# Kernel optimization log

Hardware: AMD Instinct MI355X
Metric: run time of the kernel (lower is better)

The kernel has to match this reference:

```python
import jax, jax.numpy as jnp
import numpy as np
import math

B, S, E, H = 4, 4096, 2048, 16
Dh = E // H  # 128


def setup_inputs() -> dict:
    key = jax.random.key(0)
    ks = jax.random.split(key, 8)
    s = 1.0 / math.sqrt(E)
    return {
        "x": jax.random.normal(ks[0], (B, S, E), dtype=jnp.float32),
        "Wz": jax.random.uniform(ks[1], (E, E), jnp.float32, -s, s),
        "bz": jax.random.uniform(ks[2], (E,), jnp.float32, -s, s),
        "Wx": jax.random.uniform(ks[3], (E, E), jnp.float32, -s, s),
        "bx": jax.random.uniform(ks[4], (E,), jnp.float32, -s, s),
        "phase": jax.random.normal(ks[5], (H, Dh), dtype=jnp.float32),
        "Wo": jax.random.uniform(ks[6], (E, E), jnp.float32, -s, s),
        "bo": jax.random.uniform(ks[7], (E,), jnp.float32, -s, s),
    }


def reference(x, Wz, bz, Wx, bx, phase, Wo, bo):
    # torch nn.Linear: y = x @ W.T + b  (W stored [out, in])
    z = x @ Wz.T + bz                     # [B,S,E]
    xs = x @ Wx.T + bx                    # [B,S,E]
    z_h = z.reshape(B, S, H, Dh)
    x_h = xs.reshape(B, S, H, Dh)
    # elementwise phase modulation of query heads
    mod = z_h * jnp.sin(phase)            # [B,S,H,Dh] * [H,Dh]
    # NOTE: heads are on axis -2 (no transpose to [B,H,S,Dh]),
    # so scores contract over Dh giving per-token HEAD-mixing: [B,S,H,H]
    scores = jnp.einsum('bshd,bsgd->bshg', mod, x_h) / math.sqrt(Dh)
    w = jax.nn.softmax(scores, axis=-1)   # softmax over head axis g
    att = jnp.einsum('bshg,bsgd->bshd', w, x_h)  # [B,S,H,Dh]
    att = att.reshape(B, S, E)
    return att @ Wo.T + bo
```

## Files before the change

kernel.cpp:

```cpp
#include <hip/hip_runtime.h>
#include <hip/hip_bf16.h>

#define TOK 16384
#define E 2048
#define DH 128

using bf16x8 = __attribute__((ext_vector_type(8))) __bf16;
using f32x4  = __attribute__((ext_vector_type(4))) float;
using u16x8  = __attribute__((ext_vector_type(8))) unsigned short;

static __device__ __forceinline__ unsigned short f2bf(float f) {
  union { float f; unsigned u; } x; x.f = f;
  unsigned r = x.u + 0x7fffu + ((x.u >> 16) & 1u);
  return (unsigned short)(r >> 16);
}

static __device__ __forceinline__ void gload_lds16(const unsigned short* g, unsigned short* l) {
  __builtin_amdgcn_global_load_lds(
      (const __attribute__((address_space(1))) void*)g,
      (__attribute__((address_space(3))) void*)l, 16, 0, 0);
}

__global__ __launch_bounds__(256) void cvt_plain(const float* __restrict__ in,
                                                 unsigned short* __restrict__ out, int n8) {
  int stride = gridDim.x * blockDim.x;
  for (int i = blockIdx.x * blockDim.x + threadIdx.x; i < n8; i += stride) {
    const float4* p = reinterpret_cast<const float4*>(in) + (size_t)i * 2;
    float4 v0 = p[0], v1 = p[1];
    u16x8 o;
    o[0] = f2bf(v0.x); o[1] = f2bf(v0.y); o[2] = f2bf(v0.z); o[3] = f2bf(v0.w);
    o[4] = f2bf(v1.x); o[5] = f2bf(v1.y); o[6] = f2bf(v1.z); o[7] = f2bf(v1.w);
    *(reinterpret_cast<u16x8*>(out) + i) = o;
  }
}

__global__ __launch_bounds__(256) void cvt_scaled(const float* __restrict__ in,
                                                  const float* __restrict__ phase,
                                                  unsigned short* __restrict__ out, int n8) {
  const float rs = 0.08838834764831845f;
  int stride = gridDim.x * blockDim.x;
  for (int i = blockIdx.x * blockDim.x + threadIdx.x; i < n8; i += stride) {
    int row = i >> 8;
    float sc = sinf(phase[row]) * rs;
    const float4* p = reinterpret_cast<const float4*>(in) + (size_t)i * 2;
    float4 v0 = p[0], v1 = p[1];
    u16x8 o;
    o[0] = f2bf(v0.x * sc); o[1] = f2bf(v0.y * sc); o[2] = f2bf(v0.z * sc); o[3] = f2bf(v0.w * sc);
    o[4] = f2bf(v1.x * sc); o[5] = f2bf(v1.y * sc); o[6] = f2bf(v1.z * sc); o[7] = f2bf(v1.w * sc);
    *(reinterpret_cast<u16x8*>(out) + i) = o;
  }
}

__global__ __launch_bounds__(256) void scale_bias2(const float* __restrict__ bz,
                                                   const float* __restrict__ bx,
                                                   const float* __restrict__ phase,
                                                   float* __restrict__ out) {
  const float rs = 0.08838834764831845f;
  int i = blockIdx.x * blockDim.x + threadIdx.x;
  if (i < E) out[i] = bz[i] * sinf(phase[i]) * rs;
  else if (i < 2 * E) out[i] = bx[i - E];
}

#define MFMA16 __builtin_amdgcn_mfma_f32_16x16x32_bf16

static __device__ __forceinline__ bf16x8 ldf(const unsigned short* buf, int row, int slot) {
  return *reinterpret_cast<const bf16x8*>(buf + row * 64 + ((slot ^ (row & 7)) << 3));
}

static __device__ __forceinline__ void stage_half(const unsigned short* gbase, int ld,
                                                  unsigned short* dsthalf,
                                                  int r, int slot, int wave) {
#pragma unroll
  for (int c = 0; c < 2; ++c)
    gload_lds16(gbase + (size_t)(c * 64 + r) * ld + slot * 8,
                dsthalf + c * 4096 + wave * 512);
}

static __device__ __forceinline__ void quad(f32x4 (&acc)[8][4], const bf16x8 (&a)[4][2],
                                            const bf16x8 (&b)[2][2], int mh, int nh) {
#pragma unroll
  for (int mi = 0; mi < 4; ++mi)
#pragma unroll
    for (int ni = 0; ni < 2; ++ni)
#pragma unroll
      for (int kk = 0; kk < 2; ++kk)
        acc[mh * 4 + mi][nh * 2 + ni] =
            MFMA16(a[mi][kk], b[ni][kk], acc[mh * 4 + mi][nh * 2 + ni], 0, 0, 0);
}

#define PH_BAR()  __builtin_amdgcn_s_barrier()
#define VMCNT(n)  asm volatile("s_waitcnt vmcnt(" #n ")" ::: "memory")
#define PRIO1()   __builtin_amdgcn_s_setprio(1)
#define PRIO0()   __builtin_amdgcn_s_setprio(0)

#define LD_A(dst, buf, base)                                             \
  _Pragma("unroll")                                                      \
  for (int mi = 0; mi < 4; ++mi)                                         \
    _Pragma("unroll")                                                    \
    for (int kk = 0; kk < 2; ++kk)                                       \
      dst[mi][kk] = ldf(buf, (base) + mi * 16, kk * 4 + grp);

#define LD_B(dst, buf, base)                                             \
  _Pragma("unroll")                                                      \
  for (int ni = 0; ni < 2; ++ni)                                         \
    _Pragma("unroll")                                                    \
    for (int kk = 0; kk < 2; ++kk)                                       \
      dst[ni][kk] = ldf(buf, (base) + ni * 16, kk * 4 + grp);

template <bool LAST>
static __device__ __forceinline__ void k_iter(
    const unsigned short* __restrict__ Ag, const unsigned short* __restrict__ Bg,
    int K_, int lda, int t,
    unsigned short* sA0, unsigned short* sA1, unsigned short* sB0, unsigned short* sB1,
    int r, int slot, int wave, int grp, int rA, int rB,
    bf16x8 (&bP)[2][2], bf16x8 (&bQ)[2][2], f32x4 (&acc)[8][4]) {
  const size_t k1 = (size_t)(t + 1) * 64, k2 = (size_t)(t + 2) * 64, k3 = (size_t)(t + 3) * 64;
  const size_t hA = (size_t)128 * lda, hB = (size_t)128 * K_;
  bf16x8 aF[4][2], b1F[2][2];

  LD_A(aF, sA0, rA);
  stage_half(Ag + k1, lda, sA1, r, slot, wave);
  PRIO1(); quad(acc, aF, bP, 0, 0); PRIO0();
  LD_B(b1F, sB0, rB + 32);
  stage_half(Ag + hA + k1, lda, sA1 + 8192, r, slot, wave);
  PRIO1(); quad(acc, aF, b1F, 0, 1); PRIO0();
  VMCNT(4);
  PH_BAR();

  LD_A(aF, sA0, rA + 64);
  if (!LAST) stage_half(Bg + k2, K_, sB0, r, slot, wave);
  PRIO1(); quad(acc, aF, b1F, 1, 1); PRIO0();
  LD_B(bQ, sB1, rB);
  if (!LAST) stage_half(Bg + hB + k2, K_, sB0 + 8192, r, slot, wave);
  PRIO1(); quad(acc, aF, bP, 1, 0); PRIO0();
  if (!LAST) { VMCNT(4); } else { VMCNT(0); }
  PH_BAR();

  LD_A(aF, sA1, rA);
  if (!LAST) stage_half(Ag + k2, lda, sA0, r, slot, wave);
  PRIO1(); quad(acc, aF, bQ, 0, 0); PRIO0();
  LD_B(b1F, sB1, rB + 32);
  if (!LAST) stage_half(Ag + hA + k2, lda, sA0 + 8192, r, slot, wave);
  PRIO1(); quad(acc, aF, b1F, 0, 1); PRIO0();
  if (!LAST) { VMCNT(4); }
  PH_BAR();

  LD_A(aF, sA1, rA + 64);
  if (!LAST) stage_half(Bg + k3, K_, sB1, r, slot, wave);
  PRIO1(); quad(acc, aF, b1F, 1, 1); PRIO0();
  if (!LAST) {
    LD_B(bP, sB0, rB);
    stage_half(Bg + hB + k3, K_, sB1 + 8192, r, slot, wave);
  }
  PRIO1(); quad(acc, aF, bQ, 1, 0); PRIO0();
  if (!LAST) { VMCNT(4); }
  PH_BAR();
}

template <bool OUT_BF16>
__global__ __launch_bounds__(512, 2) void gemm256(const unsigned short* __restrict__ A,
                                                  const unsigned short* __restrict__ Bm,
                                                  const float* __restrict__ bias,
                                                  void* __restrict__ C,
                                                  int M, int N, int K_, int lda) {
  extern __shared__ unsigned short lds[];
  unsigned short* sA0 = lds;
  unsigned short* sA1 = lds + 16384;
  unsigned short* sB0 = lds + 32768;
  unsigned short* sB1 = lds + 49152;

  const int nbn = N >> 8;
  const int bid = blockIdx.x;
  const int swz = (bid & 7) * ((int)gridDim.x >> 3) + (bid >> 3);
  const int by = swz / nbn, bx = swz % nbn;
  const int tm = by << 8, tn = bx << 8;

  const int tid = threadIdx.x;
  const int wave = tid >> 6, lane = tid & 63;
  const int g16 = lane & 15, grp = lane >> 4;
  const int wm = wave >> 2, wn = wave & 3;
  const int rA = wm * 128 + g16;
  const int rB = wn * 64 + g16;
  const int r = tid >> 3;
  const int slot = (tid & 7) ^ ((tid >> 3) & 7);

  const unsigned short* Ag = A + (size_t)tm * lda;
  const unsigned short* Bg = Bm + (size_t)tn * K_;
  const size_t hA = (size_t)128 * lda, hB = (size_t)128 * K_;

  f32x4 acc[8][4];
#pragma unroll
  for (int i = 0; i < 8; ++i)
#pragma unroll
    for (int j = 0; j < 4; ++j) acc[i][j] = (f32x4){0.f, 0.f, 0.f, 0.f};

  bf16x8 bP[2][2], bQ[2][2];

  stage_half(Ag, lda, sA0, r, slot, wave);
  stage_half(Ag + hA, lda, sA0 + 8192, r, slot, wave);
  stage_half(Bg, K_, sB0, r, slot, wave);
  stage_half(Bg + hB, K_, sB0 + 8192, r, slot, wave);
  stage_half(Bg + 64, K_, sB1, r, slot, wave);
  stage_half(Bg + hB + 64, K_, sB1 + 8192, r, slot, wave);
  VMCNT(4);
  __builtin_amdgcn_s_barrier();
  LD_B(bP, sB0, rB);

  const int NI = K_ >> 7;
#pragma unroll 1
  for (int i = 0; i < NI - 1; ++i)
    k_iter<false>(Ag, Bg, K_, lda, 2 * i, sA0, sA1, sB0, sB1, r, slot, wave, grp, rA, rB,
                  bP, bQ, acc);
  k_iter<true>(Ag, Bg, K_, lda, 2 * (NI - 1), sA0, sA1, sB0, sB1, r, slot, wave, grp, rA, rB,
               bP, bQ, acc);

#pragma unroll
  for (int mi = 0; mi < 8; ++mi) {
#pragma unroll
    for (int ni = 0; ni < 4; ++ni) {
      const int row = tm + wm * 128 + mi * 16 + grp * 4;
      const int col = tn + wn * 64 + ni * 16 + g16;
      const float bv = bias[col];
#pragma unroll
      for (int j = 0; j < 4; ++j) {
        const float v = acc[mi][ni][j] + bv;
        if (OUT_BF16)
          ((unsigned short*)C)[(size_t)(row + j) * N + col] = f2bf(v);
        else
          ((float*)C)[(size_t)(row + j) * N + col] = v;
      }
    }
  }
}

__global__ __launch_bounds__(256) void attn_kernel(unsigned short* zc) {
  __shared__ __align__(16) unsigned short xs_lds[4][16][136];
  __shared__ float w_lds[4][16][17];

  const int wave = threadIdx.x >> 6, lane = threadIdx.x & 63;
  const int token = (blockIdx.x << 2) | wave;
  unsigned short* modp = zc + (size_t)token * (2 * E);
  const unsigned short* xsp = modp + E;
  const int g16 = lane & 15, grp = lane >> 4;

  bf16x8 a[4], b[4];
#pragma unroll
  for (int kk = 0; kk < 4; ++kk) {
    a[kk] = *reinterpret_cast<const bf16x8*>(modp + g16 * DH + kk * 32 + grp * 8);
    b[kk] = *reinterpret_cast<const bf16x8*>(xsp  + g16 * DH + kk * 32 + grp * 8);
  }
#pragma unroll
  for (int kk = 0; kk < 4; ++kk)
    *reinterpret_cast<bf16x8*>(&xs_lds[wave][g16][kk * 32 + grp * 8]) = b[kk];

  f32x4 sc = (f32x4){0.f, 0.f, 0.f, 0.f};
#pragma unroll
  for (int kk = 0; kk < 4; ++kk)
    sc = MFMA16(a[kk], b[kk], sc, 0, 0, 0);

  float w4[4];
#pragma unroll
  for (int j = 0; j < 4; ++j) {
    float s = sc[j];
    float m = s;
#pragma unroll
    for (int off = 1; off < 16; off <<= 1) m = fmaxf(m, __shfl_xor(m, off));
    float e = __expf(s - m);
    float t = e;
#pragma unroll
    for (int off = 1; off < 16; off <<= 1) t += __shfl_xor(t, off);
    w4[j] = e / t;
  }
#pragma unroll
  for (int j = 0; j < 4; ++j) w_lds[wave][grp * 4 + j][g16] = w4[j];

  __syncthreads();

  float acc[32];
#pragma unroll
  for (int i = 0; i < 32; ++i) acc[i] = 0.f;
#pragma unroll
  for (int g = 0; g < 16; ++g) {
    const float wg = w_lds[wave][g16][g];
#pragma unroll
    for (int c = 0; c < 4; ++c) {
      bf16x8 xv = *reinterpret_cast<const bf16x8*>(&xs_lds[wave][g][grp * 32 + c * 8]);
#pragma unroll
      for (int j = 0; j < 8; ++j) acc[c * 8 + j] += wg * (float)xv[j];
    }
  }

  unsigned short* op = modp + g16 * DH + grp * 32;
#pragma unroll
  for (int c = 0; c < 4; ++c) {
    u16x8 o;
#pragma unroll
    for (int j = 0; j < 8; ++j) o[j] = f2bf(acc[c * 8 + j]);
    *reinterpret_cast<u16x8*>(op + c * 8) = o;
  }
}

extern "C" void kernel_launch(void* const* d_in, const int* in_sizes, int n_in,
                              void* d_out, int out_size, void* d_ws, size_t ws_size,
                              hipStream_t stream) {
  const float* x     = (const float*)d_in[0];
  const float* Wz    = (const float*)d_in[1];
  const float* bz    = (const float*)d_in[2];
  const float* Wx    = (const float*)d_in[3];
  const float* bx    = (const float*)d_in[4];
  const float* phase = (const float*)d_in[5];
  const float* Wo    = (const float*)d_in[6];
  const float* bo    = (const float*)d_in[7];

  char* p = (char*)d_ws;
  unsigned short* x_bf  = (unsigned short*)p; p += (size_t)TOK * E * 2;
  unsigned short* C12   = (unsigned short*)p; p += (size_t)TOK * 2 * E * 2;
  unsigned short* wzx   = (unsigned short*)p; p += (size_t)2 * E * E * 2;
  unsigned short* wo_bf = (unsigned short*)p; p += (size_t)E * E * 2;
  float* bzx            = (float*)p;          p += (size_t)2 * E * 4;

  hipFuncSetAttribute((const void*)gemm256<true>,
                      hipFuncAttributeMaxDynamicSharedMemorySize, 131072);
  hipFuncSetAttribute((const void*)gemm256<false>,
                      hipFuncAttributeMaxDynamicSharedMemorySize, 131072);

  cvt_plain<<<2048, 256, 0, stream>>>(x, x_bf, TOK * E / 8);
  cvt_scaled<<<1024, 256, 0, stream>>>(Wz, phase, wzx, E * E / 8);
  cvt_plain<<<1024, 256, 0, stream>>>(Wx, wzx + (size_t)E * E, E * E / 8);
  cvt_plain<<<1024, 256, 0, stream>>>(Wo, wo_bf, E * E / 8);
  scale_bias2<<<2 * E / 256, 256, 0, stream>>>(bz, bx, phase, bzx);

  gemm256<true><<<dim3((TOK / 256) * (2 * E / 256)), 512, 131072, stream>>>(
      x_bf, wzx, bzx, C12, TOK, 2 * E, E, E);
  attn_kernel<<<TOK / 4, 256, 0, stream>>>(C12);
  gemm256<false><<<dim3((TOK / 256) * (E / 256)), 512, 131072, stream>>>(
      C12, wo_bf, bo, (float*)d_out, TOK, E, E, 2 * E);
}
```

Measured before the change: 454.5 us.

## Shrink GEMM tiles to 256x128 with K=32 stages and 4 waves

```diff
diff --git a/kernel.cpp b/kernel.cpp
--- a/kernel.cpp
+++ b/kernel.cpp
@@ -63,29 +63,28 @@
 
 #define MFMA16 __builtin_amdgcn_mfma_f32_16x16x32_bf16
 
-static __device__ __forceinline__ bf16x8 ldf(const unsigned short* buf, int row, int slot) {
-  return *reinterpret_cast<const bf16x8*>(buf + row * 64 + ((slot ^ (row & 7)) << 3));
-}
-
-static __device__ __forceinline__ void stage_half(const unsigned short* gbase, int ld,
-                                                  unsigned short* dsthalf,
-                                                  int r, int slot, int wave) {
-#pragma unroll
-  for (int c = 0; c < 2; ++c)
-    gload_lds16(gbase + (size_t)(c * 64 + r) * ld + slot * 8,
-                dsthalf + c * 4096 + wave * 512);
-}
-
-static __device__ __forceinline__ void quad(f32x4 (&acc)[8][4], const bf16x8 (&a)[4][2],
-                                            const bf16x8 (&b)[2][2], int mh, int nh) {
+static __device__ __forceinline__ bf16x8 ldf32(const unsigned short* buf, int row, int slot) {
+  return *reinterpret_cast<const bf16x8*>(buf + row * 32 + ((slot ^ (row & 3)) << 3));
+}
+
+template <int NCH>
+static __device__ __forceinline__ void stage_tile(const unsigned short* gbase, int ld,
+                                                  unsigned short* dst,
+                                                  int srow, int s0, int wave) {
+#pragma unroll
+  for (int c = 0; c < NCH; ++c)
+    gload_lds16(gbase + (size_t)(c * 64 + srow) * ld + s0 * 8,
+                dst + c * 2048 + wave * 512);
+}
+
+static __device__ __forceinline__ void q8(f32x4 (&acc)[8][4], const bf16x8 (&a)[4],
+                                          const bf16x8 (&b)[2], int mh, int nh) {
 #pragma unroll
   for (int mi = 0; mi < 4; ++mi)
 #pragma unroll
     for (int ni = 0; ni < 2; ++ni)
-#pragma unroll
-      for (int kk = 0; kk < 2; ++kk)
-        acc[mh * 4 + mi][nh * 2 + ni] =
-            MFMA16(a[mi][kk], b[ni][kk], acc[mh * 4 + mi][nh * 2 + ni], 0, 0, 0);
+      acc[mh * 4 + mi][nh * 2 + ni] =
+          MFMA16(a[mi], b[ni], acc[mh * 4 + mi][nh * 2 + ni], 0, 0, 0);
 }
 
 #define PH_BAR()  __builtin_amdgcn_s_barrier()
@@ -93,100 +92,82 @@
 #define PRIO1()   __builtin_amdgcn_s_setprio(1)
 #define PRIO0()   __builtin_amdgcn_s_setprio(0)
 
-#define LD_A(dst, buf, base)                                             \
+#define LDA32(dst, buf, base)                                            \
   _Pragma("unroll")                                                      \
   for (int mi = 0; mi < 4; ++mi)                                         \
-    _Pragma("unroll")                                                    \
-    for (int kk = 0; kk < 2; ++kk)                                       \
-      dst[mi][kk] = ldf(buf, (base) + mi * 16, kk * 4 + grp);
-
-#define LD_B(dst, buf, base)                                             \
+    dst[mi] = ldf32(buf, (base) + mi * 16, grp);
+
+#define LDB32(dst, buf, base)                                            \
   _Pragma("unroll")                                                      \
   for (int ni = 0; ni < 2; ++ni)                                         \
-    _Pragma("unroll")                                                    \
-    for (int kk = 0; kk < 2; ++kk)                                       \
-      dst[ni][kk] = ldf(buf, (base) + ni * 16, kk * 4 + grp);
+    dst[ni] = ldf32(buf, (base) + ni * 16, grp);
 
 template <bool LAST>
 static __device__ __forceinline__ void k_iter(
     const unsigned short* __restrict__ Ag, const unsigned short* __restrict__ Bg,
     int K_, int lda, int t,
     unsigned short* sA0, unsigned short* sA1, unsigned short* sB0, unsigned short* sB1,
-    int r, int slot, int wave, int grp, int rA, int rB,
-    bf16x8 (&bP)[2][2], bf16x8 (&bQ)[2][2], f32x4 (&acc)[8][4]) {
-  const size_t k1 = (size_t)(t + 1) * 64, k2 = (size_t)(t + 2) * 64, k3 = (size_t)(t + 3) * 64;
-  const size_t hA = (size_t)128 * lda, hB = (size_t)128 * K_;
-  bf16x8 aF[4][2], b1F[2][2];
-
-  LD_A(aF, sA0, rA);
-  stage_half(Ag + k1, lda, sA1, r, slot, wave);
-  PRIO1(); quad(acc, aF, bP, 0, 0); PRIO0();
-  LD_B(b1F, sB0, rB + 32);
-  stage_half(Ag + hA + k1, lda, sA1 + 8192, r, slot, wave);
-  PRIO1(); quad(acc, aF, b1F, 0, 1); PRIO0();
-  VMCNT(4);
+    int srow, int s0, int wave, int grp, int rA, int rB, f32x4 (&acc)[8][4]) {
+  const size_t k1 = (size_t)(t + 1) * 32, k2 = (size_t)(t + 2) * 32, k3 = (size_t)(t + 3) * 32;
+  bf16x8 aF[4], b0[2], b1[2];
+
+  LDA32(aF, sA0, rA);
+  LDB32(b0, sB0, rB);
+  LDB32(b1, sB0, rB + 32);
+  stage_tile<4>(Ag + k1, lda, sA1, srow, s0, wave);
+  PRIO1(); q8(acc, aF, b0, 0, 0); q8(acc, aF, b1, 0, 1); PRIO0();
   PH_BAR();
 
-  LD_A(aF, sA0, rA + 64);
-  if (!LAST) stage_half(Bg + k2, K_, sB0, r, slot, wave);
-  PRIO1(); quad(acc, aF, b1F, 1, 1); PRIO0();
-  LD_B(bQ, sB1, rB);
-  if (!LAST) stage_half(Bg + hB + k2, K_, sB0 + 8192, r, slot, wave);
-  PRIO1(); quad(acc, aF, bP, 1, 0); PRIO0();
-  if (!LAST) { VMCNT(4); } else { VMCNT(0); }
+  LDA32(aF, sA0, rA + 64);
+  if (!LAST) stage_tile<2>(Bg + k2, K_, sB0, srow, s0, wave);
+  PRIO1(); q8(acc, aF, b1, 1, 1); q8(acc, aF, b0, 1, 0); PRIO0();
+  if (!LAST) { VMCNT(2); } else { VMCNT(0); }
   PH_BAR();
 
-  LD_A(aF, sA1, rA);
-  if (!LAST) stage_half(Ag + k2, lda, sA0, r, slot, wave);
-  PRIO1(); quad(acc, aF, bQ, 0, 0); PRIO0();
-  LD_B(b1F, sB1, rB + 32);
-  if (!LAST) stage_half(Ag + hA + k2, lda, sA0 + 8192, r, slot, wave);
-  PRIO1(); quad(acc, aF, b1F, 0, 1); PRIO0();
-  if (!LAST) { VMCNT(4); }
+  LDA32(aF, sA1, rA);
+  LDB32(b0, sB1, rB);
+  LDB32(b1, sB1, rB + 32);
+  if (!LAST) stage_tile<4>(Ag + k2, lda, sA0, srow, s0, wave);
+  PRIO1(); q8(acc, aF, b0, 0, 0); q8(acc, aF, b1, 0, 1); PRIO0();
   PH_BAR();
 
-  LD_A(aF, sA1, rA + 64);
-  if (!LAST) stage_half(Bg + k3, K_, sB1, r, slot, wave);
-  PRIO1(); quad(acc, aF, b1F, 1, 1); PRIO0();
-  if (!LAST) {
-    LD_B(bP, sB0, rB);
-    stage_half(Bg + hB + k3, K_, sB1 + 8192, r, slot, wave);
-  }
-  PRIO1(); quad(acc, aF, bQ, 1, 0); PRIO0();
-  if (!LAST) { VMCNT(4); }
+  LDA32(aF, sA1, rA + 64);
+  if (!LAST) stage_tile<2>(Bg + k3, K_, sB1, srow, s0, wave);
+  PRIO1(); q8(acc, aF, b1, 1, 1); q8(acc, aF, b0, 1, 0); PRIO0();
+  if (!LAST) { VMCNT(2); }
   PH_BAR();
 }
 
 template <bool OUT_BF16>
-__global__ __launch_bounds__(512, 2) void gemm256(const unsigned short* __restrict__ A,
+__global__ __launch_bounds__(256, 2) void gemm256(const unsigned short* __restrict__ A,
                                                   const unsigned short* __restrict__ Bm,
                                                   const float* __restrict__ bias,
                                                   void* __restrict__ C,
                                                   int M, int N, int K_, int lda) {
   extern __shared__ unsigned short lds[];
   unsigned short* sA0 = lds;
-  unsigned short* sA1 = lds + 16384;
-  unsigned short* sB0 = lds + 32768;
-  unsigned short* sB1 = lds + 49152;
-
-  const int nbn = N >> 8;
+  unsigned short* sA1 = lds + 8192;
+  unsigned short* sB0 = lds + 16384;
+  unsigned short* sB1 = lds + 20480;
+
+  const int nbn = N >> 7;
   const int bid = blockIdx.x;
   const int swz = (bid & 7) * ((int)gridDim.x >> 3) + (bid >> 3);
   const int by = swz / nbn, bx = swz % nbn;
-  const int tm = by << 8, tn = bx << 8;
+  const int tm = by << 8, tn = bx << 7;
 
   const int tid = threadIdx.x;
   const int wave = tid >> 6, lane = tid & 63;
   const int g16 = lane & 15, grp = lane >> 4;
-  const int wm = wave >> 2, wn = wave & 3;
+  const int wm = wave >> 1, wn = wave & 1;
   const int rA = wm * 128 + g16;
   const int rB = wn * 64 + g16;
-  const int r = tid >> 3;
-  const int slot = (tid & 7) ^ ((tid >> 3) & 7);
+  const int srow = tid >> 2;
+  const int s0 = (tid & 3) ^ (srow & 3);
 
   const unsigned short* Ag = A + (size_t)tm * lda;
   const unsigned short* Bg = Bm + (size_t)tn * K_;
-  const size_t hA = (size_t)128 * lda, hB = (size_t)128 * K_;
+  const size_t hA2 = (size_t)0;
 
   f32x4 acc[8][4];
 #pragma unroll
@@ -194,25 +175,18 @@
 #pragma unroll
     for (int j = 0; j < 4; ++j) acc[i][j] = (f32x4){0.f, 0.f, 0.f, 0.f};
 
-  bf16x8 bP[2][2], bQ[2][2];
-
-  stage_half(Ag, lda, sA0, r, slot, wave);
-  stage_half(Ag + hA, lda, sA0 + 8192, r, slot, wave);
-  stage_half(Bg, K_, sB0, r, slot, wave);
-  stage_half(Bg + hB, K_, sB0 + 8192, r, slot, wave);
-  stage_half(Bg + 64, K_, sB1, r, slot, wave);
-  stage_half(Bg + hB + 64, K_, sB1 + 8192, r, slot, wave);
-  VMCNT(4);
+  (void)hA2;
+  stage_tile<4>(Ag, lda, sA0, srow, s0, wave);
+  stage_tile<2>(Bg, K_, sB0, srow, s0, wave);
+  stage_tile<2>(Bg + 32, K_, sB1, srow, s0, wave);
+  VMCNT(2);
   __builtin_amdgcn_s_barrier();
-  LD_B(bP, sB0, rB);
-
-  const int NI = K_ >> 7;
+
+  const int NI = K_ >> 6;
 #pragma unroll 1
   for (int i = 0; i < NI - 1; ++i)
-    k_iter<false>(Ag, Bg, K_, lda, 2 * i, sA0, sA1, sB0, sB1, r, slot, wave, grp, rA, rB,
-                  bP, bQ, acc);
-  k_iter<true>(Ag, Bg, K_, lda, 2 * (NI - 1), sA0, sA1, sB0, sB1, r, slot, wave, grp, rA, rB,
-               bP, bQ, acc);
+    k_iter<false>(Ag, Bg, K_, lda, 2 * i, sA0, sA1, sB0, sB1, srow, s0, wave, grp, rA, rB, acc);
+  k_iter<true>(Ag, Bg, K_, lda, 2 * (NI - 1), sA0, sA1, sB0, sB1, srow, s0, wave, grp, rA, rB, acc);
 
 #pragma unroll
   for (int mi = 0; mi < 8; ++mi) {
@@ -319,20 +293,15 @@
   unsigned short* wo_bf = (unsigned short*)p; p += (size_t)E * E * 2;
   float* bzx            = (float*)p;          p += (size_t)2 * E * 4;
 
-  hipFuncSetAttribute((const void*)gemm256<true>,
-                      hipFuncAttributeMaxDynamicSharedMemorySize, 131072);
-  hipFuncSetAttribute((const void*)gemm256<false>,
-                      hipFuncAttributeMaxDynamicSharedMemorySize, 131072);
-
   cvt_plain<<<2048, 256, 0, stream>>>(x, x_bf, TOK * E / 8);
   cvt_scaled<<<1024, 256, 0, stream>>>(Wz, phase, wzx, E * E / 8);
   cvt_plain<<<1024, 256, 0, stream>>>(Wx, wzx + (size_t)E * E, E * E / 8);
   cvt_plain<<<1024, 256, 0, stream>>>(Wo, wo_bf, E * E / 8);
   scale_bias2<<<2 * E / 256, 256, 0, stream>>>(bz, bx, phase, bzx);
 
-  gemm256<true><<<dim3((TOK / 256) * (2 * E / 256)), 512, 131072, stream>>>(
+  gemm256<true><<<dim3((TOK / 256) * (2 * E / 128)), 256, 49152, stream>>>(
       x_bf, wzx, bzx, C12, TOK, 2 * E, E, E);
   attn_kernel<<<TOK / 4, 256, 0, stream>>>(C12);
-  gemm256<false><<<dim3((TOK / 256) * (E / 256)), 512, 131072, stream>>>(
+  gemm256<false><<<dim3((TOK / 256) * (E / 128)), 256, 49152, stream>>>(
       C12, wo_bf, bo, (float*)d_out, TOK, E, E, 2 * E);
 }
```

New measurement: 530.8 us. 1.17x slower.
